# Kernel tuning notes

Hardware: AMD Instinct MI355X
Metric: run time of the kernel (lower is better)

Reference implementation:

```python
import jax, jax.numpy as jnp
import numpy as np

N_NODES = 50000
N_EDGES = 800000


def _gcn_conv(x, W, b, src, dst, deg_inv_sqrt, n_nodes):
    # PyG GCNConv: h = x @ W, then symmetric-normalized sum aggregation
    h = x @ W  # [N, F_out]
    norm = deg_inv_sqrt[src] * deg_inv_sqrt[dst]  # [E_aug]
    msg = h[src] * norm[:, None]  # [E_aug, F_out]
    out = jax.ops.segment_sum(msg, dst, num_segments=n_nodes)
    return out + b


def setup_inputs() -> dict:
    key = jax.random.key(0)
    k1, k2, k3, k4 = jax.random.split(key, 4)
    x = jax.random.normal(k1, (N_NODES, 128), dtype=jnp.float32)
    edge_index = jax.random.randint(k2, (2, N_EDGES), 0, N_NODES, dtype=jnp.int64)
    W1 = jax.random.normal(k3, (128, 64), dtype=jnp.float32) * (1.0 / np.sqrt(128))
    b1 = jnp.zeros((64,), dtype=jnp.float32)
    W2 = jax.random.normal(k4, (64, 32), dtype=jnp.float32) * (1.0 / np.sqrt(64))
    b2 = jnp.zeros((32,), dtype=jnp.float32)
    return {"x": x, "edge_index": edge_index, "W1": W1, "b1": b1, "W2": W2, "b2": b2}


def reference(x, edge_index, W1, b1, W2, b2):
    n_nodes = x.shape[0]
    # add self-loops (PyG GCNConv default)
    loop = jnp.arange(n_nodes, dtype=edge_index.dtype)
    src = jnp.concatenate([edge_index[0], loop])
    dst = jnp.concatenate([edge_index[1], loop])
    # symmetric normalization: deg from target index (gcn_norm)
    deg = jax.ops.segment_sum(jnp.ones_like(dst, dtype=x.dtype), dst, num_segments=n_nodes)
    deg_inv_sqrt = jnp.where(deg > 0, jax.lax.rsqrt(jnp.maximum(deg, 1.0)), 0.0)

    h = _gcn_conv(x, W1, b1, src, dst, deg_inv_sqrt, n_nodes)
    h = jax.nn.relu(h)
    # dropout is identity in eval mode (reference runs inference)
    out = _gcn_conv(h, W2, b2, src, dst, deg_inv_sqrt, n_nodes)
    return out
```

## Files before the change

### kernel.cpp

```cpp
#include <hip/hip_runtime.h>
#include <hip/hip_fp16.h>


#define F_IN 128
#define F_MID 64
#define F_OUT 32
#define NBLK 256

#define RFL(x) __builtin_amdgcn_readfirstlane(x)

__device__ __forceinline__ void h8acc(float* a, const uint4& v) {
    const __half2* hp = (const __half2*)&v;
#pragma unroll
    for (int i = 0; i < 4; ++i) {
        float2 f = __half22float2(hp[i]);
        a[2 * i]     += f.x;
        a[2 * i + 1] += f.y;
    }
}

__device__ __forceinline__ void h8unpack(float* f, const uint4& v) {
    const __half2* hp = (const __half2*)&v;
#pragma unroll
    for (int i = 0; i < 4; ++i) {
        float2 t = __half22float2(hp[i]);
        f[2 * i]     = t.x;
        f[2 * i + 1] = t.y;
    }
}

__device__ __forceinline__ uint4 pack8(const float4& a, const float4& b) {
    union { uint4 u; __half2 h[4]; } pk;
    pk.h[0] = __float22half2_rn(make_float2(a.x, a.y));
    pk.h[1] = __float22half2_rn(make_float2(a.z, a.w));
    pk.h[2] = __float22half2_rn(make_float2(b.x, b.y));
    pk.h[3] = __float22half2_rn(make_float2(b.z, b.w));
    return pk.u;
}

__global__ __launch_bounds__(256) void k_hist(
    const int* __restrict__ dst, int E, int chunk, int nbuk,
    int* __restrict__ blockHist) {
    __shared__ int cnt[256];
    int t = threadIdx.x;
    cnt[t] = 0;
    __syncthreads();
    int e0 = blockIdx.x * chunk;
    int e1 = min(E, e0 + chunk);
    for (int e = e0 + t; e < e1; e += 256)
        atomicAdd(&cnt[dst[e] >> 8], 1);
    __syncthreads();
    if (t < nbuk) blockHist[blockIdx.x * nbuk + t] = cnt[t];
}

__global__ __launch_bounds__(NBLK) void k_scan_buckets(
    const int* __restrict__ blockHist, int nbuk,
    int* __restrict__ blockOff, int* __restrict__ bucketTotal) {
    __shared__ int s[NBLK];
    int b = blockIdx.x;
    int t = threadIdx.x;
    int v = blockHist[t * nbuk + b];
    s[t] = v;
    __syncthreads();
    for (int o = 1; o < NBLK; o <<= 1) {
        int add = (t >= o) ? s[t - o] : 0;
        __syncthreads();
        s[t] += add;
        __syncthreads();
    }
    blockOff[t * nbuk + b] = s[t] - v;
    if (t == NBLK - 1) bucketTotal[b] = s[t];
}

__global__ __launch_bounds__(256) void k_scan_starts(
    const int* __restrict__ bucketTotal, int nbuk, int E,
    int* __restrict__ bucketStart) {
    __shared__ int s[256];
    int t = threadIdx.x;
    int v = (t < nbuk) ? bucketTotal[t] : 0;
    s[t] = v;
    __syncthreads();
    for (int o = 1; o < 256; o <<= 1) {
        int add = (t >= o) ? s[t - o] : 0;
        __syncthreads();
        s[t] += add;
        __syncthreads();
    }
    if (t < nbuk) bucketStart[t] = s[t] - v;
    if (t == 0) bucketStart[nbuk] = E;
}

__global__ __launch_bounds__(256) void k_scatter_edges(
    const int* __restrict__ src, const int* __restrict__ dst, int E, int chunk,
    int nbuk, const int* __restrict__ blockOff, const int* __restrict__ bucketStart,
    int* __restrict__ esort) {
    __shared__ int off[256];
    int t = threadIdx.x;
    if (t < nbuk) off[t] = blockOff[blockIdx.x * nbuk + t] + bucketStart[t];
    __syncthreads();
    int e0 = blockIdx.x * chunk;
    int e1 = min(E, e0 + chunk);
    for (int e = e0 + t; e < e1; e += 256) {
        int d = dst[e];
        int pos = atomicAdd(&off[d >> 8], 1);
        esort[pos] = (src[e] << 8) | (d & 255);
    }
}

__global__ __launch_bounds__(256) void k_bucket_csr(
    const int* __restrict__ esort, const int* __restrict__ bucketStart, int n,
    int* __restrict__ rowstart, int* __restrict__ deg, float* __restrict__ dis,
    int* __restrict__ col) {
    __shared__ int cnt[256];
    __shared__ int s[256];
    __shared__ int cur[256];
    int b = blockIdx.x;
    int t = threadIdx.x;
    int node0 = b << 8;
    int e0 = bucketStart[b], e1 = bucketStart[b + 1];
    cnt[t] = 0;
    __syncthreads();
    for (int e = e0 + t; e < e1; e += 256)
        atomicAdd(&cnt[esort[e] & 255], 1);
    __syncthreads();
    int v = cnt[t];
    s[t] = v;
    __syncthreads();
    for (int o = 1; o < 256; o <<= 1) {
        int add = (t >= o) ? s[t - o] : 0;
        __syncthreads();
        s[t] += add;
        __syncthreads();
    }
    int ex = s[t] - v;
    cur[t] = ex;
    int node = node0 + t;
    if (node < n) {
        rowstart[node] = e0 + ex;
        deg[node] = v;
        dis[node] = rsqrtf((float)(v + 1));
    }
    __syncthreads();
    for (int e = e0 + t; e < e1; e += 256) {
        int p = esort[e];
        int pos = atomicAdd(&cur[p & 255], 1);
        col[e0 + pos] = p >> 8;
    }
}

__global__ __launch_bounds__(256, 4) void k_gemm1(
    const float* __restrict__ x, const float* __restrict__ W1,
    const float* __restrict__ dis, uint4* __restrict__ g1h, int n) {
    __shared__ float xs[64 * 129];
    int tid  = threadIdx.x;
    int row0 = blockIdx.x * 64;
    for (int i = tid; i < 64 * F_IN; i += 256) {
        int r = i >> 7, k = i & 127;
        int gr = row0 + r;
        xs[r * 129 + k] = (gr < n) ? x[(size_t)gr * F_IN + k] : 0.0f;
    }
    __syncthreads();
    int w = RFL(tid >> 6);
    int r = tid & 63;
    const float4* W4 = (const float4*)W1;
    float4 a0 = {0.f,0.f,0.f,0.f}, a1 = a0, a2 = a0, a3 = a0;
#pragma unroll 4
    for (int k = 0; k < F_IN; ++k) {
        float xv = xs[r * 129 + k];
        float4 w0 = W4[k * 16 + w * 4 + 0];
        float4 w1 = W4[k * 16 + w * 4 + 1];
        float4 w2 = W4[k * 16 + w * 4 + 2];
        float4 w3 = W4[k * 16 + w * 4 + 3];
        a0.x += xv * w0.x; a0.y += xv * w0.y; a0.z += xv * w0.z; a0.w += xv * w0.w;
        a1.x += xv * w1.x; a1.y += xv * w1.y; a1.z += xv * w1.z; a1.w += xv * w1.w;
        a2.x += xv * w2.x; a2.y += xv * w2.y; a2.z += xv * w2.z; a2.w += xv * w2.w;
        a3.x += xv * w3.x; a3.y += xv * w3.y; a3.z += xv * w3.z; a3.w += xv * w3.w;
    }
    int gr = row0 + r;
    if (gr < n) {
        float dv = dis[gr];
        a0.x *= dv; a0.y *= dv; a0.z *= dv; a0.w *= dv;
        a1.x *= dv; a1.y *= dv; a1.z *= dv; a1.w *= dv;
        a2.x *= dv; a2.y *= dv; a2.z *= dv; a2.w *= dv;
        a3.x *= dv; a3.y *= dv; a3.z *= dv; a3.w *= dv;
        g1h[(size_t)gr * 8 + w * 2 + 0] = pack8(a0, a1);
        g1h[(size_t)gr * 8 + w * 2 + 1] = pack8(a2, a3);
    }
}

__global__ __launch_bounds__(256) void k_gather1(
    const int* __restrict__ rowstart, const int* __restrict__ deg,
    const int* __restrict__ col, const uint4* __restrict__ g1h,
    const float* __restrict__ dis, const float* __restrict__ b1,
    uint4* __restrict__ h16, int n) {
    int wave = RFL(threadIdx.x >> 6);
    int lane = threadIdx.x & 63;
    int q    = lane & 7;
    int slot = lane >> 3;
    int d    = blockIdx.x * 4 + wave;
    if (d >= n) return;
    int base = RFL(rowstart[d]);
    int cnt  = RFL(deg[d]);
    float a[8] = {0,0,0,0,0,0,0,0};
    float b[8] = {0,0,0,0,0,0,0,0};
    if (slot == 0) {
        uint4 v = g1h[(size_t)d * 8 + q];
        h8acc(a, v);
    }
    int j = 0;
    for (; j + 32 <= cnt; j += 32) {
        int s0 = col[base + j + slot];
        int s1 = col[base + j + 8 + slot];
        int s2 = col[base + j + 16 + slot];
        int s3 = col[base + j + 24 + slot];
        uint4 v0 = g1h[(size_t)s0 * 8 + q];
        uint4 v1 = g1h[(size_t)s1 * 8 + q];
        uint4 v2 = g1h[(size_t)s2 * 8 + q];
        uint4 v3 = g1h[(size_t)s3 * 8 + q];
        h8acc(a, v0); h8acc(b, v1); h8acc(a, v2); h8acc(b, v3);
    }
    for (; j + 16 <= cnt; j += 16) {
        int s0 = col[base + j + slot];
        int s1 = col[base + j + 8 + slot];
        uint4 v0 = g1h[(size_t)s0 * 8 + q];
        uint4 v1 = g1h[(size_t)s1 * 8 + q];
        h8acc(a, v0); h8acc(b, v1);
    }
    for (; j + 8 <= cnt; j += 8) {
        int s = col[base + j + slot];
        uint4 v = g1h[(size_t)s * 8 + q];
        h8acc(a, v);
    }
    if (slot < cnt - j) {
        int s = col[base + j + slot];
        uint4 v = g1h[(size_t)s * 8 + q];
        h8acc(a, v);
    }
#pragma unroll
    for (int i = 0; i < 8; ++i) a[i] += b[i];
#pragma unroll
    for (int i = 0; i < 8; ++i) a[i] += __shfl_xor(a[i], 8);
#pragma unroll
    for (int i = 0; i < 8; ++i) a[i] += __shfl_xor(a[i], 16);
#pragma unroll
    for (int i = 0; i < 8; ++i) a[i] += __shfl_xor(a[i], 32);
    if (slot == 0) {
        float dv = dis[d];
        float4 bv0 = ((const float4*)b1)[q * 2 + 0];
        float4 bv1 = ((const float4*)b1)[q * 2 + 1];
        float4 o0, o1;
        o0.x = fmaxf(a[0] * dv + bv0.x, 0.f);
        o0.y = fmaxf(a[1] * dv + bv0.y, 0.f);
        o0.z = fmaxf(a[2] * dv + bv0.z, 0.f);
        o0.w = fmaxf(a[3] * dv + bv0.w, 0.f);
        o1.x = fmaxf(a[4] * dv + bv1.x, 0.f);
        o1.y = fmaxf(a[5] * dv + bv1.y, 0.f);
        o1.z = fmaxf(a[6] * dv + bv1.z, 0.f);
        o1.w = fmaxf(a[7] * dv + bv1.w, 0.f);
        h16[(size_t)d * 8 + q] = pack8(o0, o1);
    }
}

__global__ __launch_bounds__(256, 4) void k_gemm2(
    const uint4* __restrict__ h16, const float* __restrict__ W2,
    const float* __restrict__ dis, uint4* __restrict__ g2h, int n) {
    __shared__ float hs[64 * 65];
    int tid  = threadIdx.x;
    int row0 = blockIdx.x * 64;
    for (int i = tid; i < 64 * 8; i += 256) {
        int r = i >> 3, q = i & 7;
        int gr = row0 + r;
        float f[8] = {0,0,0,0,0,0,0,0};
        if (gr < n) {
            uint4 v = h16[(size_t)gr * 8 + q];
            h8unpack(f, v);
        }
        float* p = &hs[r * 65 + q * 8];
#pragma unroll
        for (int k = 0; k < 8; ++k) p[k] = f[k];
    }
    __syncthreads();
    int w = RFL(tid >> 6);
    int r = tid & 63;
    const float4* W4 = (const float4*)W2;
    float4 a0 = {0.f,0.f,0.f,0.f}, a1 = a0;
#pragma unroll 4
    for (int k = 0; k < F_MID; ++k) {
        float hv = hs[r * 65 + k];
        float4 w0 = W4[k * 8 + w * 2 + 0];
        float4 w1 = W4[k * 8 + w * 2 + 1];
        a0.x += hv * w0.x; a0.y += hv * w0.y; a0.z += hv * w0.z; a0.w += hv * w0.w;
        a1.x += hv * w1.x; a1.y += hv * w1.y; a1.z += hv * w1.z; a1.w += hv * w1.w;
    }
    int gr = row0 + r;
    if (gr < n) {
        float dv = dis[gr];
        a0.x *= dv; a0.y *= dv; a0.z *= dv; a0.w *= dv;
        a1.x *= dv; a1.y *= dv; a1.z *= dv; a1.w *= dv;
        g2h[(size_t)gr * 4 + w] = pack8(a0, a1);
    }
}

__global__ __launch_bounds__(256) void k_gather2(
    const int* __restrict__ rowstart, const int* __restrict__ deg,
    const int* __restrict__ col, const uint4* __restrict__ g2h,
    const float* __restrict__ dis, const float* __restrict__ b2,
    float* __restrict__ out, int n) {
    int wave = RFL(threadIdx.x >> 6);
    int lane = threadIdx.x & 63;
    int q    = lane & 3;
    int slot = lane >> 2;
    int d    = blockIdx.x * 4 + wave;
    if (d >= n) return;
    int base = RFL(rowstart[d]);
    int cnt  = RFL(deg[d]);
    float a[8] = {0,0,0,0,0,0,0,0};
    float b[8] = {0,0,0,0,0,0,0,0};
    if (slot == 0) {
        uint4 v = g2h[(size_t)d * 4 + q];
        h8acc(a, v);
    }
    int j = 0;
    for (; j + 64 <= cnt; j += 64) {
        int s0 = col[base + j + slot];
        int s1 = col[base + j + 16 + slot];
        int s2 = col[base + j + 32 + slot];
        int s3 = col[base + j + 48 + slot];
        uint4 v0 = g2h[(size_t)s0 * 4 + q];
        uint4 v1 = g2h[(size_t)s1 * 4 + q];
        uint4 v2 = g2h[(size_t)s2 * 4 + q];
        uint4 v3 = g2h[(size_t)s3 * 4 + q];
        h8acc(a, v0); h8acc(b, v1); h8acc(a, v2); h8acc(b, v3);
    }
    for (; j + 32 <= cnt; j += 32) {
        int s0 = col[base + j + slot];
        int s1 = col[base + j + 16 + slot];
        uint4 v0 = g2h[(size_t)s0 * 4 + q];
        uint4 v1 = g2h[(size_t)s1 * 4 + q];
        h8acc(a, v0); h8acc(b, v1);
    }
    for (; j + 16 <= cnt; j += 16) {
        int s = col[base + j + slot];
        uint4 v = g2h[(size_t)s * 4 + q];
        h8acc(a, v);
    }
    if (slot < cnt - j) {
        int s = col[base + j + slot];
        uint4 v = g2h[(size_t)s * 4 + q];
        h8acc(a, v);
    }
#pragma unroll
    for (int i = 0; i < 8; ++i) a[i] += b[i];
#pragma unroll
    for (int i = 0; i < 8; ++i) a[i] += __shfl_xor(a[i], 4);
#pragma unroll
    for (int i = 0; i < 8; ++i) a[i] += __shfl_xor(a[i], 8);
#pragma unroll
    for (int i = 0; i < 8; ++i) a[i] += __shfl_xor(a[i], 16);
#pragma unroll
    for (int i = 0; i < 8; ++i) a[i] += __shfl_xor(a[i], 32);
    if (slot == 0) {
        float dv = dis[d];
        float4 bv0 = ((const float4*)b2)[q * 2 + 0];
        float4 bv1 = ((const float4*)b2)[q * 2 + 1];
        float4 o0, o1;
        o0.x = a[0] * dv + bv0.x;
        o0.y = a[1] * dv + bv0.y;
        o0.z = a[2] * dv + bv0.z;
        o0.w = a[3] * dv + bv0.w;
        o1.x = a[4] * dv + bv1.x;
        o1.y = a[5] * dv + bv1.y;
        o1.z = a[6] * dv + bv1.z;
        o1.w = a[7] * dv + bv1.w;
        float4* O4 = (float4*)out;
        O4[(size_t)d * 8 + q * 2 + 0] = o0;
        O4[(size_t)d * 8 + q * 2 + 1] = o1;
    }
}

extern "C" void kernel_launch(void* const* d_in, const int* in_sizes, int n_in,
                              void* d_out, int out_size, void* d_ws, size_t ws_size,
                              hipStream_t stream) {
    const float* x  = (const float*)d_in[0];
    const int*   ei = (const int*)d_in[1];
    const float* W1 = (const float*)d_in[2];
    const float* b1 = (const float*)d_in[3];
    const float* W2 = (const float*)d_in[4];
    const float* b2 = (const float*)d_in[5];

    int n = in_sizes[0] / F_IN;
    int E = in_sizes[1] / 2;
    const int* src = ei;
    const int* dst = ei + E;

    int nbuk  = (n + 255) >> 8;
    int chunk = (E + NBLK - 1) / NBLK;

    char* ws = (char*)d_ws;
    size_t off = 0;
    auto alloc = [&](size_t bytes) {
        char* p = ws + off;
        off += (bytes + 255) & ~(size_t)255;
        return p;
    };
    int*   blockHist   = (int*)  alloc((size_t)NBLK * nbuk * 4);
    int*   blockOff    = (int*)  alloc((size_t)NBLK * nbuk * 4);
    int*   bucketTotal = (int*)  alloc((size_t)nbuk * 4);
    int*   bucketStart = (int*)  alloc((size_t)(nbuk + 1) * 4);
    int*   esort       = (int*)  alloc((size_t)E * 4);
    int*   col         = (int*)  alloc((size_t)E * 4);
    int*   rowstart    = (int*)  alloc((size_t)n * 4);
    int*   deg         = (int*)  alloc((size_t)n * 4);
    float* dis         = (float*)alloc((size_t)n * 4);
    uint4* g1h         = (uint4*)alloc((size_t)n * F_MID * 2);
    uint4* h16         = (uint4*)alloc((size_t)n * F_MID * 2);
    uint4* g2h         = (uint4*)alloc((size_t)n * F_OUT * 2);

    k_hist<<<NBLK, 256, 0, stream>>>(dst, E, chunk, nbuk, blockHist);
    k_scan_buckets<<<nbuk, NBLK, 0, stream>>>(blockHist, nbuk, blockOff, bucketTotal);
    k_scan_starts<<<1, 256, 0, stream>>>(bucketTotal, nbuk, E, bucketStart);
    k_scatter_edges<<<NBLK, 256, 0, stream>>>(src, dst, E, chunk, nbuk, blockOff,
                                              bucketStart, esort);
    k_bucket_csr<<<nbuk, 256, 0, stream>>>(esort, bucketStart, n, rowstart, deg, dis, col);

    k_gemm1<<<(n + 63) / 64, 256, 0, stream>>>(x, W1, dis, g1h, n);
    k_gather1<<<(n + 3) / 4, 256, 0, stream>>>(rowstart, deg, col, g1h, dis, b1, h16, n);
    k_gemm2<<<(n + 63) / 64, 256, 0, stream>>>(h16, W2, dis, g2h, n);
    k_gather2<<<(n + 3) / 4, 256, 0, stream>>>(rowstart, deg, col, g2h, dis, b2,
                                               (float*)d_out, n);
}
```

Before: 182.4 us.

## Fuse edge bucketing into one pass and fold layer-2 GEMM into gather1

```diff
diff --git a/kernel.cpp b/kernel.cpp
--- a/kernel.cpp
+++ b/kernel.cpp
@@ -6,6 +6,7 @@
 #define F_MID 64
 #define F_OUT 32
 #define NBLK 256
+#define CAP 8192
 
 #define RFL(x) __builtin_amdgcn_readfirstlane(x)
 
@@ -16,16 +17,6 @@
         float2 f = __half22float2(hp[i]);
         a[2 * i]     += f.x;
         a[2 * i + 1] += f.y;
-    }
-}
-
-__device__ __forceinline__ void h8unpack(float* f, const uint4& v) {
-    const __half2* hp = (const __half2*)&v;
-#pragma unroll
-    for (int i = 0; i < 4; ++i) {
-        float2 t = __half22float2(hp[i]);
-        f[2 * i]     = t.x;
-        f[2 * i + 1] = t.y;
     }
 }
 
@@ -38,10 +29,11 @@
     return pk.u;
 }
 
-__global__ __launch_bounds__(256) void k_hist(
-    const int* __restrict__ dst, int E, int chunk, int nbuk,
-    int* __restrict__ blockHist) {
+__global__ __launch_bounds__(256) void k_build_scatter(
+    const int* __restrict__ src, const int* __restrict__ dst, int E, int chunk,
+    int nbuk, int* __restrict__ cursor, int* __restrict__ esort) {
     __shared__ int cnt[256];
+    __shared__ int off[256];
     int t = threadIdx.x;
     cnt[t] = 0;
     __syncthreads();
@@ -50,56 +42,11 @@
     for (int e = e0 + t; e < e1; e += 256)
         atomicAdd(&cnt[dst[e] >> 8], 1);
     __syncthreads();
-    if (t < nbuk) blockHist[blockIdx.x * nbuk + t] = cnt[t];
-}
-
-__global__ __launch_bounds__(NBLK) void k_scan_buckets(
-    const int* __restrict__ blockHist, int nbuk,
-    int* __restrict__ blockOff, int* __restrict__ bucketTotal) {
-    __shared__ int s[NBLK];
-    int b = blockIdx.x;
-    int t = threadIdx.x;
-    int v = blockHist[t * nbuk + b];
-    s[t] = v;
-    __syncthreads();
-    for (int o = 1; o < NBLK; o <<= 1) {
-        int add = (t >= o) ? s[t - o] : 0;
-        __syncthreads();
-        s[t] += add;
-        __syncthreads();
-    }
-    blockOff[t * nbuk + b] = s[t] - v;
-    if (t == NBLK - 1) bucketTotal[b] = s[t];
-}
-
-__global__ __launch_bounds__(256) void k_scan_starts(
-    const int* __restrict__ bucketTotal, int nbuk, int E,
-    int* __restrict__ bucketStart) {
-    __shared__ int s[256];
-    int t = threadIdx.x;
-    int v = (t < nbuk) ? bucketTotal[t] : 0;
-    s[t] = v;
-    __syncthreads();
-    for (int o = 1; o < 256; o <<= 1) {
-        int add = (t >= o) ? s[t - o] : 0;
-        __syncthreads();
-        s[t] += add;
-        __syncthreads();
-    }
-    if (t < nbuk) bucketStart[t] = s[t] - v;
-    if (t == 0) bucketStart[nbuk] = E;
-}
-
-__global__ __launch_bounds__(256) void k_scatter_edges(
-    const int* __restrict__ src, const int* __restrict__ dst, int E, int chunk,
-    int nbuk, const int* __restrict__ blockOff, const int* __restrict__ bucketStart,
-    int* __restrict__ esort) {
-    __shared__ int off[256];
-    int t = threadIdx.x;
-    if (t < nbuk) off[t] = blockOff[blockIdx.x * nbuk + t] + bucketStart[t];
-    __syncthreads();
-    int e0 = blockIdx.x * chunk;
-    int e1 = min(E, e0 + chunk);
+    if (t < nbuk) {
+        int c = cnt[t];
+        off[t] = t * CAP + (c ? atomicAdd(&cursor[t], c) : 0);
+    }
+    __syncthreads();
     for (int e = e0 + t; e < e1; e += 256) {
         int d = dst[e];
         int pos = atomicAdd(&off[d >> 8], 1);
@@ -108,7 +55,7 @@
 }
 
 __global__ __launch_bounds__(256) void k_bucket_csr(
-    const int* __restrict__ esort, const int* __restrict__ bucketStart, int n,
+    const int* __restrict__ esort, const int* __restrict__ cursor, int n,
     int* __restrict__ rowstart, int* __restrict__ deg, float* __restrict__ dis,
     int* __restrict__ col) {
     __shared__ int cnt[256];
@@ -117,7 +64,8 @@
     int b = blockIdx.x;
     int t = threadIdx.x;
     int node0 = b << 8;
-    int e0 = bucketStart[b], e1 = bucketStart[b + 1];
+    int e0 = b * CAP;
+    int e1 = e0 + cursor[b];
     cnt[t] = 0;
     __syncthreads();
     for (int e = e0 + t; e < e1; e += 256)
@@ -188,116 +136,92 @@
     }
 }
 
-__global__ __launch_bounds__(256) void k_gather1(
+__global__ __launch_bounds__(256) void k_gather1_g2(
     const int* __restrict__ rowstart, const int* __restrict__ deg,
     const int* __restrict__ col, const uint4* __restrict__ g1h,
     const float* __restrict__ dis, const float* __restrict__ b1,
-    uint4* __restrict__ h16, int n) {
-    int wave = RFL(threadIdx.x >> 6);
-    int lane = threadIdx.x & 63;
+    const float* __restrict__ W2, __half* __restrict__ g2h, int n) {
+    __shared__ float W2s[F_MID * F_OUT];
+    __shared__ float hrow[4 * F_MID];
+    int t = threadIdx.x;
+    for (int i = t; i < F_MID * F_OUT; i += 256) W2s[i] = W2[i];
+    __syncthreads();
+    int wave = RFL(t >> 6);
+    int lane = t & 63;
     int q    = lane & 7;
     int slot = lane >> 3;
     int d    = blockIdx.x * 4 + wave;
-    if (d >= n) return;
-    int base = RFL(rowstart[d]);
-    int cnt  = RFL(deg[d]);
-    float a[8] = {0,0,0,0,0,0,0,0};
-    float b[8] = {0,0,0,0,0,0,0,0};
-    if (slot == 0) {
-        uint4 v = g1h[(size_t)d * 8 + q];
-        h8acc(a, v);
-    }
-    int j = 0;
-    for (; j + 32 <= cnt; j += 32) {
-        int s0 = col[base + j + slot];
-        int s1 = col[base + j + 8 + slot];
-        int s2 = col[base + j + 16 + slot];
-        int s3 = col[base + j + 24 + slot];
-        uint4 v0 = g1h[(size_t)s0 * 8 + q];
-        uint4 v1 = g1h[(size_t)s1 * 8 + q];
-        uint4 v2 = g1h[(size_t)s2 * 8 + q];
-        uint4 v3 = g1h[(size_t)s3 * 8 + q];
-        h8acc(a, v0); h8acc(b, v1); h8acc(a, v2); h8acc(b, v3);
-    }
-    for (; j + 16 <= cnt; j += 16) {
-        int s0 = col[base + j + slot];
-        int s1 = col[base + j + 8 + slot];
-        uint4 v0 = g1h[(size_t)s0 * 8 + q];
-        uint4 v1 = g1h[(size_t)s1 * 8 + q];
-        h8acc(a, v0); h8acc(b, v1);
-    }
-    for (; j + 8 <= cnt; j += 8) {
-        int s = col[base + j + slot];
-        uint4 v = g1h[(size_t)s * 8 + q];
-        h8acc(a, v);
-    }
-    if (slot < cnt - j) {
-        int s = col[base + j + slot];
-        uint4 v = g1h[(size_t)s * 8 + q];
-        h8acc(a, v);
-    }
-#pragma unroll
-    for (int i = 0; i < 8; ++i) a[i] += b[i];
-#pragma unroll
-    for (int i = 0; i < 8; ++i) a[i] += __shfl_xor(a[i], 8);
-#pragma unroll
-    for (int i = 0; i < 8; ++i) a[i] += __shfl_xor(a[i], 16);
-#pragma unroll
-    for (int i = 0; i < 8; ++i) a[i] += __shfl_xor(a[i], 32);
-    if (slot == 0) {
+    if (d < n) {
+        int base = RFL(rowstart[d]);
+        int cnt  = RFL(deg[d]);
+        float a[8] = {0,0,0,0,0,0,0,0};
+        float b[8] = {0,0,0,0,0,0,0,0};
+        if (slot == 0) {
+            uint4 v = g1h[(size_t)d * 8 + q];
+            h8acc(a, v);
+        }
+        int j = 0;
+        for (; j + 32 <= cnt; j += 32) {
+            int s0 = col[base + j + slot];
+            int s1 = col[base + j + 8 + slot];
+            int s2 = col[base + j + 16 + slot];
+            int s3 = col[base + j + 24 + slot];
+            uint4 v0 = g1h[(size_t)s0 * 8 + q];
+            uint4 v1 = g1h[(size_t)s1 * 8 + q];
+            uint4 v2 = g1h[(size_t)s2 * 8 + q];
+            uint4 v3 = g1h[(size_t)s3 * 8 + q];
+            h8acc(a, v0); h8acc(b, v1); h8acc(a, v2); h8acc(b, v3);
+        }
+        for (; j + 16 <= cnt; j += 16) {
+            int s0 = col[base + j + slot];
+            int s1 = col[base + j + 8 + slot];
+            uint4 v0 = g1h[(size_t)s0 * 8 + q];
+            uint4 v1 = g1h[(size_t)s1 * 8 + q];
+            h8acc(a, v0); h8acc(b, v1);
+        }
+        for (; j + 8 <= cnt; j += 8) {
+            int s = col[base + j + slot];
+            uint4 v = g1h[(size_t)s * 8 + q];
+            h8acc(a, v);
+        }
+        if (slot < cnt - j) {
+            int s = col[base + j + slot];
+            uint4 v = g1h[(size_t)s * 8 + q];
+            h8acc(a, v);
+        }
+#pragma unroll
+        for (int i = 0; i < 8; ++i) a[i] += b[i];
+#pragma unroll
+        for (int i = 0; i < 8; ++i) a[i] += __shfl_xor(a[i], 8);
+#pragma unroll
+        for (int i = 0; i < 8; ++i) a[i] += __shfl_xor(a[i], 16);
+#pragma unroll
+        for (int i = 0; i < 8; ++i) a[i] += __shfl_xor(a[i], 32);
         float dv = dis[d];
-        float4 bv0 = ((const float4*)b1)[q * 2 + 0];
-        float4 bv1 = ((const float4*)b1)[q * 2 + 1];
-        float4 o0, o1;
-        o0.x = fmaxf(a[0] * dv + bv0.x, 0.f);
-        o0.y = fmaxf(a[1] * dv + bv0.y, 0.f);
-        o0.z = fmaxf(a[2] * dv + bv0.z, 0.f);
-        o0.w = fmaxf(a[3] * dv + bv0.w, 0.f);
-        o1.x = fmaxf(a[4] * dv + bv1.x, 0.f);
-        o1.y = fmaxf(a[5] * dv + bv1.y, 0.f);
-        o1.z = fmaxf(a[6] * dv + bv1.z, 0.f);
-        o1.w = fmaxf(a[7] * dv + bv1.w, 0.f);
-        h16[(size_t)d * 8 + q] = pack8(o0, o1);
-    }
-}
-
-__global__ __launch_bounds__(256, 4) void k_gemm2(
-    const uint4* __restrict__ h16, const float* __restrict__ W2,
-    const float* __restrict__ dis, uint4* __restrict__ g2h, int n) {
-    __shared__ float hs[64 * 65];
-    int tid  = threadIdx.x;
-    int row0 = blockIdx.x * 64;
-    for (int i = tid; i < 64 * 8; i += 256) {
-        int r = i >> 3, q = i & 7;
-        int gr = row0 + r;
-        float f[8] = {0,0,0,0,0,0,0,0};
-        if (gr < n) {
-            uint4 v = h16[(size_t)gr * 8 + q];
-            h8unpack(f, v);
-        }
-        float* p = &hs[r * 65 + q * 8];
-#pragma unroll
-        for (int k = 0; k < 8; ++k) p[k] = f[k];
-    }
-    __syncthreads();
-    int w = RFL(tid >> 6);
-    int r = tid & 63;
-    const float4* W4 = (const float4*)W2;
-    float4 a0 = {0.f,0.f,0.f,0.f}, a1 = a0;
-#pragma unroll 4
-    for (int k = 0; k < F_MID; ++k) {
-        float hv = hs[r * 65 + k];
-        float4 w0 = W4[k * 8 + w * 2 + 0];
-        float4 w1 = W4[k * 8 + w * 2 + 1];
-        a0.x += hv * w0.x; a0.y += hv * w0.y; a0.z += hv * w0.z; a0.w += hv * w0.w;
-        a1.x += hv * w1.x; a1.y += hv * w1.y; a1.z += hv * w1.z; a1.w += hv * w1.w;
-    }
-    int gr = row0 + r;
-    if (gr < n) {
-        float dv = dis[gr];
-        a0.x *= dv; a0.y *= dv; a0.z *= dv; a0.w *= dv;
-        a1.x *= dv; a1.y *= dv; a1.z *= dv; a1.w *= dv;
-        g2h[(size_t)gr * 4 + w] = pack8(a0, a1);
+        if (slot == 0) {
+            float4 bv0 = ((const float4*)b1)[q * 2 + 0];
+            float4 bv1 = ((const float4*)b1)[q * 2 + 1];
+            float* hp = &hrow[wave * F_MID + q * 8];
+            hp[0] = fmaxf(a[0] * dv + bv0.x, 0.f);
+            hp[1] = fmaxf(a[1] * dv + bv0.y, 0.f);
+            hp[2] = fmaxf(a[2] * dv + bv0.z, 0.f);
+            hp[3] = fmaxf(a[3] * dv + bv0.w, 0.f);
+            hp[4] = fmaxf(a[4] * dv + bv1.x, 0.f);
+            hp[5] = fmaxf(a[5] * dv + bv1.y, 0.f);
+            hp[6] = fmaxf(a[6] * dv + bv1.z, 0.f);
+            hp[7] = fmaxf(a[7] * dv + bv1.w, 0.f);
+        }
+        int jo = lane & 31;
+        int kh = lane >> 5;
+        float acc2 = 0.f;
+        const float* hb = &hrow[wave * F_MID + kh * 32];
+        const float* wb = &W2s[kh * 32 * F_OUT + jo];
+#pragma unroll 8
+        for (int k = 0; k < 32; ++k)
+            acc2 += hb[k] * wb[k * F_OUT];
+        acc2 += __shfl_xor(acc2, 32);
+        if (lane < 32)
+            g2h[(size_t)d * F_OUT + jo] = __float2half(acc2 * dv);
     }
 }
 
@@ -403,29 +327,22 @@
         off += (bytes + 255) & ~(size_t)255;
         return p;
     };
-    int*   blockHist   = (int*)  alloc((size_t)NBLK * nbuk * 4);
-    int*   blockOff    = (int*)  alloc((size_t)NBLK * nbuk * 4);
-    int*   bucketTotal = (int*)  alloc((size_t)nbuk * 4);
-    int*   bucketStart = (int*)  alloc((size_t)(nbuk + 1) * 4);
-    int*   esort       = (int*)  alloc((size_t)E * 4);
-    int*   col         = (int*)  alloc((size_t)E * 4);
-    int*   rowstart    = (int*)  alloc((size_t)n * 4);
-    int*   deg         = (int*)  alloc((size_t)n * 4);
-    float* dis         = (float*)alloc((size_t)n * 4);
-    uint4* g1h         = (uint4*)alloc((size_t)n * F_MID * 2);
-    uint4* h16         = (uint4*)alloc((size_t)n * F_MID * 2);
-    uint4* g2h         = (uint4*)alloc((size_t)n * F_OUT * 2);
-
-    k_hist<<<NBLK, 256, 0, stream>>>(dst, E, chunk, nbuk, blockHist);
-    k_scan_buckets<<<nbuk, NBLK, 0, stream>>>(blockHist, nbuk, blockOff, bucketTotal);
-    k_scan_starts<<<1, 256, 0, stream>>>(bucketTotal, nbuk, E, bucketStart);
-    k_scatter_edges<<<NBLK, 256, 0, stream>>>(src, dst, E, chunk, nbuk, blockOff,
-                                              bucketStart, esort);
-    k_bucket_csr<<<nbuk, 256, 0, stream>>>(esort, bucketStart, n, rowstart, deg, dis, col);
+    int*    cursor   = (int*)   alloc((size_t)nbuk * 4);
+    int*    esort    = (int*)   alloc((size_t)nbuk * CAP * 4);
+    int*    col      = (int*)   alloc((size_t)nbuk * CAP * 4);
+    int*    rowstart = (int*)   alloc((size_t)n * 4);
+    int*    deg      = (int*)   alloc((size_t)n * 4);
+    float*  dis      = (float*) alloc((size_t)n * 4);
+    uint4*  g1h      = (uint4*) alloc((size_t)n * F_MID * 2);
+    __half* g2h      = (__half*)alloc((size_t)n * F_OUT * 2);
+
+    hipMemsetAsync(cursor, 0, (size_t)nbuk * 4, stream);
+    k_build_scatter<<<NBLK, 256, 0, stream>>>(src, dst, E, chunk, nbuk, cursor, esort);
+    k_bucket_csr<<<nbuk, 256, 0, stream>>>(esort, cursor, n, rowstart, deg, dis, col);
 
     k_gemm1<<<(n + 63) / 64, 256, 0, stream>>>(x, W1, dis, g1h, n);
-    k_gather1<<<(n + 3) / 4, 256, 0, stream>>>(rowstart, deg, col, g1h, dis, b1, h16, n);
-    k_gemm2<<<(n + 63) / 64, 256, 0, stream>>>(h16, W2, dis, g2h, n);
-    k_gather2<<<(n + 3) / 4, 256, 0, stream>>>(rowstart, deg, col, g2h, dis, b2,
-                                               (float*)d_out, n);
-}
+    k_gather1_g2<<<(n + 3) / 4, 256, 0, stream>>>(rowstart, deg, col, g1h, dis, b1,
+                                                  W2, g2h, n);
+    k_gather2<<<(n + 3) / 4, 256, 0, stream>>>(rowstart, deg, col, (const uint4*)g2h,
+                                               dis, b2, (float*)d_out, n);
+}
```

New measurement: 189.2 us. 1.04x slower.
